# Performance work log

Hardware: AMD Instinct MI355X
Metric: run time of the kernel (lower is better)

## Reference

```python
import math
import jax, jax.numpy as jnp
import numpy as np

B, A, M, NC = 32, 8400, 32, 80
TOP_K, ALPHA, BETA, EPS = 13, 1.0, 6.0, 1e-9
IMG = 640.0


def _ciou(b1, b2, eps=1e-7):
    # b1, b2 broadcastable [..., 4]; CIoU as in compute_iou (box1=gt, box2=pred)
    b1x1, b1y1, b1x2, b1y2 = b1[..., 0], b1[..., 1], b1[..., 2], b1[..., 3]
    b2x1, b2y1, b2x2, b2y2 = b2[..., 0], b2[..., 1], b2[..., 2], b2[..., 3]
    w1, h1 = b1x2 - b1x1, b1y2 - b1y1 + eps
    w2, h2 = b2x2 - b2x1, b2y2 - b2y1 + eps
    inter = (jnp.minimum(b1x2, b2x2) - jnp.maximum(b1x1, b2x1)).clip(0) * \
            (jnp.minimum(b1y2, b2y2) - jnp.maximum(b1y1, b2y1)).clip(0)
    union = w1 * h1 + w2 * h2 - inter + eps
    iou = inter / union
    cw = jnp.maximum(b1x2, b2x2) - jnp.minimum(b1x1, b2x1)
    ch = jnp.maximum(b1y2, b2y2) - jnp.minimum(b1y1, b2y1)
    c2 = cw ** 2 + ch ** 2 + eps
    rho2 = ((b2x1 + b2x2 - b1x1 - b1x2) ** 2 + (b2y1 + b2y2 - b1y1 - b1y2) ** 2) / 4.0
    v = (4.0 / math.pi ** 2) * (jnp.arctan(w2 / h2) - jnp.arctan(w1 / h1)) ** 2
    alpha = jax.lax.stop_gradient(v / (v - iou + (1.0 + eps)))
    return iou - (rho2 / c2 + v * alpha)


def setup_inputs() -> dict:
    key = jax.random.key(0)
    ks = jax.random.split(key, 8)
    pd_scores = jax.random.uniform(ks[0], (B, A, NC), jnp.float32)
    anc_points = jax.random.uniform(ks[1], (A, 2), jnp.float32) * IMG
    # predicted boxes around anchor points (valid x1<x2, y1<y2)
    off = jax.random.uniform(ks[2], (B, A, 4), jnp.float32) * 80.0 + 2.0
    pd_bboxes = jnp.concatenate([anc_points[None] - off[..., :2],
                                 anc_points[None] + off[..., 2:]], -1)
    # GT boxes: random centers and sizes, clipped to image
    c = jax.random.uniform(ks[3], (B, M, 2), jnp.float32) * IMG
    wh = jax.random.uniform(ks[4], (B, M, 2), jnp.float32) * 180.0 + 20.0
    gt_bboxes = jnp.concatenate([(c - wh / 2).clip(0, IMG), (c + wh / 2).clip(0, IMG)], -1)
    gt_labels = jax.random.randint(ks[5], (B, M, 1), 0, NC, jnp.int64)
    n_valid = jax.random.randint(ks[6], (B,), 1, M + 1)
    mask_gt = (jnp.arange(M)[None, :] < n_valid[:, None]).astype(jnp.float32)[..., None]
    return {"pd_scores": pd_scores, "pd_bboxes": pd_bboxes, "anc_points": anc_points,
            "gt_labels": gt_labels, "gt_bboxes": gt_bboxes, "mask_gt": mask_gt}


def reference(pd_scores, pd_bboxes, anc_points, gt_labels, gt_bboxes, mask_gt):
    b, a, nc = pd_scores.shape
    m = gt_bboxes.shape[1]
    dtype = pd_scores.dtype

    # anchors-inside-GT mask: [B,M,A]
    lt = gt_bboxes[:, :, None, :2]          # [B,M,1,2]
    rb = gt_bboxes[:, :, None, 2:]
    deltas = jnp.concatenate([anc_points[None, None] - lt,
                              rb - anc_points[None, None]], -1)  # [B,M,A,4]
    mask_in_gts = deltas.min(-1) > EPS
    mg = mask_gt[..., 0] > 0                 # [B,M] bool
    gt_mask = mask_in_gts & mg[:, :, None]

    # per-GT class score gather: pd_scores[b, :, gt_labels[b,m]] -> [B,M,A]
    labels = gt_labels[..., 0]               # [B,M]
    idx = jnp.broadcast_to(labels[:, :, None, None], (b, m, a, 1))
    gathered = jnp.take_along_axis(jnp.broadcast_to(pd_scores[:, None], (b, m, a, nc)), idx, axis=3)[..., 0]
    bbox_scores = jnp.where(gt_mask, gathered, 0.0)

    # CIoU overlaps (dense, masked) [B,M,A]
    iou = _ciou(gt_bboxes[:, :, None, :], pd_bboxes[:, None, :, :])
    overlaps = jnp.where(gt_mask, jnp.maximum(iou, 0.0), 0.0)

    align_metric = bbox_scores ** ALPHA * overlaps ** BETA

    # top-k selection with duplicate suppression (faithful to scatter_add loop)
    _, tk_idx = jax.lax.top_k(align_metric, TOP_K)      # [B,M,K]
    tk_mask = jnp.broadcast_to(mg[:, :, None], tk_idx.shape)
    tk_idx = jnp.where(tk_mask, tk_idx, 0)
    bi = jnp.arange(b)[:, None, None]
    mi = jnp.arange(m)[None, :, None]
    counts = jnp.zeros((b, m, a), jnp.int32).at[bi, mi, tk_idx].add(1)
    mask_top_k = jnp.where(counts > 1, 0, counts).astype(dtype)

    mask_pos = mask_top_k * mask_in_gts.astype(dtype) * mg[:, :, None].astype(dtype)
    fg_mask = mask_pos.sum(1)                            # [B,A]

    # resolve anchors assigned to multiple GTs (no-op when none; matches torch branch)
    mask_multi = fg_mask[:, None, :] > 1                 # [B,M,A] (broadcast)
    max_idx = overlaps.argmax(1)                         # [B,A]
    is_max = (jnp.arange(m)[None, :, None] == max_idx[:, None, :]).astype(dtype)
    mask_pos = jnp.where(mask_multi, is_max, mask_pos)
    fg_mask = mask_pos.sum(1)

    target_gt_idx = mask_pos.argmax(1)                   # [B,A]
    target_labels = jnp.maximum(jnp.take_along_axis(labels, target_gt_idx, axis=1), 0)
    target_bboxes = jnp.take_along_axis(
        gt_bboxes, jnp.broadcast_to(target_gt_idx[..., None], (b, a, 4)), axis=1)

    target_scores = jax.nn.one_hot(target_labels, NC, dtype=dtype)
    target_scores = jnp.where((fg_mask > 0)[..., None], target_scores, 0.0)

    am = align_metric * mask_pos
    pos_am = am.max(-1, keepdims=True)                   # [B,M,1]
    pos_ov = (overlaps * mask_pos).max(-1, keepdims=True)
    norm = (am * pos_ov / (pos_am + EPS)).max(1)[..., None]  # [B,A,1]
    target_scores = target_scores * norm

    return target_bboxes, target_scores, fg_mask > 0
```

## Files before the change

### kernel.cpp

```cpp
#include <hip/hip_runtime.h>
#include <math.h>

#define BB 32
#define AA 8400
#define MM 32
#define NCC 80
#define TOPK 13
#define CAP 1024
#define NW (AA / 32 + 1)

typedef float nfloat4 __attribute__((ext_vector_type(4)));

__device__ __forceinline__ void wave_argmax(float& v, int& i) {
    #pragma unroll
    for (int off = 32; off > 0; off >>= 1) {
        float ov = __shfl_xor(v, off, 64);
        int oi = __shfl_xor(i, off, 64);
        if (ov > v || (ov == v && oi < i)) { v = ov; i = oi; }
    }
}

__global__ __launch_bounds__(256) void k12_topk(
        const float* __restrict__ pd_scores, const float* __restrict__ pd_bboxes,
        const float* __restrict__ anc, const int* __restrict__ gt_labels,
        const float* __restrict__ gt_bboxes, const float* __restrict__ mask_gt,
        int* __restrict__ sel_idx, float* __restrict__ pos_am, float* __restrict__ pos_ov) {
    __shared__ float lval[CAP];
    __shared__ int   lidx[CAP];
    __shared__ unsigned int bmask[NW];
    __shared__ float wv[4];
    __shared__ int   wi[4];
    __shared__ int   wsum[4];
    __shared__ int   s_p, s_sel;
    const float eps = 1e-7f;
    int bm = blockIdx.x;
    int b = bm >> 5;
    int tid = threadIdx.x;
    int lane = tid & 63;
    int wid = tid >> 6;
    if (tid == 0) pos_am[bm] = 0.f;
    if (tid == 1) pos_ov[bm] = 0.f;
    if (tid == 2) s_p = 0;
    if (tid == 3) s_sel = 0;
    if (tid < 16) sel_idx[bm * 16 + tid] = -1;
    if (!(mask_gt[bm] > 0.f)) return;

    for (int i = tid; i < NW; i += 256) bmask[i] = 0u;
    float4 g = reinterpret_cast<const float4*>(gt_bboxes)[bm];

    const float4* anc4 = reinterpret_cast<const float4*>(anc);
    unsigned long long bits = 0ull;
    int c_t = 0;
    #pragma unroll
    for (int j = 0; j < 17; j++) {
        int e = tid + (j << 8);
        if (e < 4200) {
            float4 an = anc4[e];
            float d0 = fminf(fminf(an.x - g.x, an.y - g.y), fminf(g.z - an.x, g.w - an.y));
            float d1 = fminf(fminf(an.z - g.x, an.w - g.y), fminf(g.z - an.z, g.w - an.w));
            if (d0 > 1e-9f) { bits |= 1ull << (2 * j);     c_t++; }
            if (d1 > 1e-9f) { bits |= 1ull << (2 * j + 1); c_t++; }
        }
    }
    int x = c_t;
    #pragma unroll
    for (int off = 1; off < 64; off <<= 1) {
        int y = __shfl_up(x, off, 64);
        if (lane >= off) x += y;
    }
    if (lane == 63) wsum[wid] = x;
    __syncthreads();
    int base = 0;
    #pragma unroll
    for (int w = 0; w < 4; w++) if (w < wid) base += wsum[w];
    int n_c = min(wsum[0] + wsum[1] + wsum[2] + wsum[3], CAP);
    {
        int o = base + x - c_t;
        unsigned long long mm_ = bits;
        while (mm_) {
            int k = __builtin_ctzll(mm_);
            mm_ &= mm_ - 1ull;
            int i = 2 * tid + 512 * (k >> 1) + (k & 1);
            if (o < CAP) lidx[o] = i;
            o++;
        }
    }
    for (int s = n_c + tid; s < CAP; s += 256) { lval[s] = -1.f; lidx[s] = AA; }
    __syncthreads();

    float w1 = g.z - g.x, h1 = g.w - g.y + eps;
    float atg = atanf(w1 / h1);
    float w1h1 = w1 * h1;
    float sgx = g.x + g.z, sgy = g.y + g.w;
    int lab = gt_labels[bm];
    const float4* pbb = reinterpret_cast<const float4*>(pd_bboxes) + (long)b * AA;
    const float* scp = pd_scores + (long)b * AA * NCC + lab;
    int nit = (n_c + 255) >> 8;
    for (int it = 0; it < nit; it++) {
        int s = (it << 8) + tid;
        bool pos = false;
        if (s < n_c) {
            int i = lidx[s];
            float4 pb = pbb[i];
            float sc = scp[(long)i * NCC];
            float w2 = pb.z - pb.x, h2 = pb.w - pb.y + eps;
            float iw = fmaxf(fminf(g.z, pb.z) - fmaxf(g.x, pb.x), 0.f);
            float ih = fmaxf(fminf(g.w, pb.w) - fmaxf(g.y, pb.y), 0.f);
            float inter = iw * ih;
            float uni = w1h1 + w2 * h2 - inter + eps;
            float iou = inter / uni;
            float cw = fmaxf(g.z, pb.z) - fminf(g.x, pb.x);
            float ch = fmaxf(g.w, pb.w) - fminf(g.y, pb.y);
            float c2 = cw * cw + ch * ch + eps;
            float dx = pb.x + pb.z - sgx, dy = pb.y + pb.w - sgy;
            float rho2 = (dx * dx + dy * dy) * 0.25f;
            float dv = atanf(w2 / h2) - atg;
            float v = 0.4052847345693511f * dv * dv;
            float alpha = v / (v - iou + (1.0f + eps));
            float cv = iou - (rho2 / c2 + v * alpha);
            float ov = fmaxf(cv, 0.f);
            float o2 = ov * ov;
            float val = sc * o2 * o2 * o2;
            pos = val > 0.f;
            lval[s] = pos ? val : -1.f;
            if (pos) atomicOr(&bmask[i >> 5], 1u << (i & 31));
        }
        unsigned long long pm = __ballot(pos);
        if (lane == 0) atomicAdd(&s_p, (int)__popcll(pm));
    }
    __syncthreads();
    int p = s_p;

    if (p >= TOPK) {
        float v0 = lval[tid], v1 = lval[tid + 256], v2 = lval[tid + 512], v3 = lval[tid + 768];
        int   i0 = lidx[tid], i1 = lidx[tid + 256], i2 = lidx[tid + 512], i3 = lidx[tid + 768];
        int mysel = -1;
        for (int k = 0; k < TOPK; k++) {
            float bv = v0; int bi = i0;
            if (v1 > bv || (v1 == bv && i1 < bi)) { bv = v1; bi = i1; }
            if (v2 > bv || (v2 == bv && i2 < bi)) { bv = v2; bi = i2; }
            if (v3 > bv || (v3 == bv && i3 < bi)) { bv = v3; bi = i3; }
            wave_argmax(bv, bi);
            if (lane == 0) { wv[wid] = bv; wi[wid] = bi; }
            __syncthreads();
            float gv = wv[0]; int gi = wi[0];
            #pragma unroll
            for (int w = 1; w < 4; w++) {
                float ov = wv[w]; int oi = wi[w];
                if (ov > gv || (ov == gv && oi < gi)) { gv = ov; gi = oi; }
            }
            if (tid == k) mysel = gi;
            if (i0 == gi) v0 = -1.f;
            if (i1 == gi) v1 = -1.f;
            if (i2 == gi) v2 = -1.f;
            if (i3 == gi) v3 = -1.f;
            __syncthreads();
        }
        if (tid < TOPK) sel_idx[bm * 16 + tid] = mysel;
    } else {
        for (int s = tid; s < n_c; s += 256)
            if (lval[s] > 0.f) {
                int slot = atomicAdd(&s_sel, 1);
                sel_idx[bm * 16 + slot] = lidx[s];
            }
        if (wid == 0) {
            int need = TOPK - p;
            for (int base_i = 0; need > 0 && base_i < AA; base_i += 64) {
                int i = base_i + lane;
                bool cand = (i < AA) && !((bmask[i >> 5] >> (i & 31)) & 1u);
                unsigned long long wm = __ballot(cand);
                int take = min(need, (int)__popcll(wm));
                if (cand && (int)__popcll(wm & ((1ull << lane) - 1ull)) < take) {
                    float2 an = reinterpret_cast<const float2*>(anc)[i];
                    float dmin = fminf(fminf(an.x - g.x, an.y - g.y), fminf(g.z - an.x, g.w - an.y));
                    if (dmin > 1e-9f) {
                        int slot = atomicAdd(&s_sel, 1);
                        sel_idx[bm * 16 + slot] = i;
                    }
                }
                need -= take;
            }
        }
    }
}

__global__ __launch_bounds__(256) void k3_resolve(
        const float* __restrict__ pd_scores, const float* __restrict__ pd_bboxes,
        const float* __restrict__ anc, const int* __restrict__ gt_labels,
        const float* __restrict__ gt_bboxes, const float* __restrict__ mask_gt,
        const int* __restrict__ sel_idx,
        float* __restrict__ pos_am, float* __restrict__ pos_ov,
        float* __restrict__ out_bbox, float* __restrict__ out_fg,
        int2* __restrict__ meta) {
    __shared__ float sg[MM][8];
    __shared__ int slab[MM];
    __shared__ int smg[MM];
    __shared__ unsigned int selcol[256];
    const float eps = 1e-7f;
    int b = blockIdx.y;
    int tid = threadIdx.x;
    if (tid < MM) {
        int gm = b * MM + tid;
        float4 g = reinterpret_cast<const float4*>(gt_bboxes)[gm];
        float w1 = g.z - g.x, h1 = g.w - g.y + eps;
        sg[tid][0] = g.x; sg[tid][1] = g.y; sg[tid][2] = g.z; sg[tid][3] = g.w;
        sg[tid][4] = w1 * h1;
        sg[tid][5] = atanf(w1 / h1);
        sg[tid][6] = g.x + g.z;
        sg[tid][7] = g.y + g.w;
        int lb = gt_labels[gm]; if (lb < 0) lb = 0;
        slab[tid] = lb;
        smg[tid] = mask_gt[gm] > 0.f ? 1 : 0;
    }
    selcol[tid] = 0u;
    __syncthreads();
    int a0 = blockIdx.x * 256;
    const int* sl = sel_idx + b * MM * 16;
    #pragma unroll
    for (int t = tid; t < MM * 16; t += 256) {
        int e = sl[t];
        if (e >= a0 && e < a0 + 256) atomicOr(&selcol[e - a0], 1u << (t >> 4));
    }
    __syncthreads();
    int a = a0 + tid;
    if (a >= AA) return;
    int g = b * AA + a;
    unsigned int sel = selcol[tid];
    int fg = __popc(sel);

    int tg = 0; bool fgo = false; float ovt = 0.f;
    if (fg >= 1) {
        float ax = anc[a * 2], ay = anc[a * 2 + 1];
        float4 pb = reinterpret_cast<const float4*>(pd_bboxes)[g];
        float w2 = pb.z - pb.x, h2 = pb.w - pb.y + eps;
        float atp = atanf(w2 / h2);
        float w2h2 = w2 * h2;
        float spx = pb.x + pb.z, spy = pb.y + pb.w;
        fgo = true;
        if (fg == 1) {
            tg = __ffs(sel) - 1;
            float gx1 = sg[tg][0], gy1 = sg[tg][1], gx2 = sg[tg][2], gy2 = sg[tg][3];
            float iw = fmaxf(fminf(gx2, pb.z) - fmaxf(gx1, pb.x), 0.f);
            float ih = fmaxf(fminf(gy2, pb.w) - fmaxf(gy1, pb.y), 0.f);
            float inter = iw * ih;
            float uni = sg[tg][4] + w2h2 - inter + eps;
            float iou = inter / uni;
            float cw = fmaxf(gx2, pb.z) - fminf(gx1, pb.x);
            float ch = fmaxf(gy2, pb.w) - fminf(gy1, pb.y);
            float c2 = cw * cw + ch * ch + eps;
            float dx = spx - sg[tg][6], dy = spy - sg[tg][7];
            float rho2 = (dx * dx + dy * dy) * 0.25f;
            float dv = atp - sg[tg][5];
            float v = 0.4052847345693511f * dv * dv;
            float alpha = v / (v - iou + (1.0f + eps));
            ovt = fmaxf(iou - (rho2 / c2 + v * alpha), 0.f);
        } else {
            float bestov = -1.f; int bestm = 0;
            for (int mm = 0; mm < MM; mm++) {
                float gx1 = sg[mm][0], gy1 = sg[mm][1], gx2 = sg[mm][2], gy2 = sg[mm][3];
                float dmin = fminf(fminf(ax - gx1, ay - gy1), fminf(gx2 - ax, gy2 - ay));
                float ov = 0.f;
                if ((dmin > 1e-9f) && smg[mm]) {
                    float iw = fmaxf(fminf(gx2, pb.z) - fmaxf(gx1, pb.x), 0.f);
                    float ih = fmaxf(fminf(gy2, pb.w) - fmaxf(gy1, pb.y), 0.f);
                    float inter = iw * ih;
                    float uni = sg[mm][4] + w2h2 - inter + eps;
                    float iou = inter / uni;
                    float cw = fmaxf(gx2, pb.z) - fminf(gx1, pb.x);
                    float ch = fmaxf(gy2, pb.w) - fminf(gy1, pb.y);
                    float c2 = cw * cw + ch * ch + eps;
                    float dx = spx - sg[mm][6], dy = spy - sg[mm][7];
                    float rho2 = (dx * dx + dy * dy) * 0.25f;
                    float dv = atp - sg[mm][5];
                    float v = 0.4052847345693511f * dv * dv;
                    float alpha = v / (v - iou + (1.0f + eps));
                    ov = fmaxf(iou - (rho2 / c2 + v * alpha), 0.f);
                }
                if (ov > bestov) { bestov = ov; bestm = mm; }
            }
            tg = bestm; ovt = bestov;
        }
    }

    nfloat4 gb = {sg[tg][0], sg[tg][1], sg[tg][2], sg[tg][3]};
    __builtin_nontemporal_store(gb, reinterpret_cast<nfloat4*>(out_bbox) + g);
    out_fg[g] = fgo ? 1.f : 0.f;
    float amv = 0.f;
    if (fgo) {
        float sc = pd_scores[(long)g * NCC + slab[tg]];
        float o2 = ovt * ovt;
        amv = sc * o2 * o2 * o2;
        atomicMax((int*)&pos_am[b * MM + tg], __float_as_int(amv));
        atomicMax((int*)&pos_ov[b * MM + tg], __float_as_int(ovt));
    }
    meta[g] = make_int2(__float_as_int(amv), tg | (slab[tg] << 8) | ((fgo ? 1 : 0) << 16));
}

__global__ __launch_bounds__(256) void k4_scores(
        const int2* __restrict__ meta,
        const float* __restrict__ pos_am, const float* __restrict__ pos_ov,
        float* __restrict__ out_scores) {
    int g = blockIdx.x * 256 + threadIdx.x;
    const int NQ = NCC / 4;
    if (g >= BB * AA * NQ) return;
    int ba = g / NQ;
    int c0 = (g % NQ) * 4;
    nfloat4 o = {0.f, 0.f, 0.f, 0.f};
    int2 mt = meta[ba];
    int p = mt.y;
    if (p & (1 << 16)) {
        int tg = p & 31, lab = (p >> 8) & 127;
        int b = ba / AA;
        int bm = b * MM + tg;
        float nv = (__int_as_float(mt.x) * pos_ov[bm]) / (pos_am[bm] + 1e-9f);
        int d = lab - c0;
        if (d == 0) o.x = nv; else if (d == 1) o.y = nv;
        else if (d == 2) o.z = nv; else if (d == 3) o.w = nv;
    }
    __builtin_nontemporal_store(o, reinterpret_cast<nfloat4*>(out_scores) + g);
}

extern "C" void kernel_launch(void* const* d_in, const int* in_sizes, int n_in,
                              void* d_out, int out_size, void* d_ws, size_t ws_size,
                              hipStream_t stream) {
    const float* pd_scores = (const float*)d_in[0];
    const float* pd_bboxes = (const float*)d_in[1];
    const float* anc       = (const float*)d_in[2];
    const int*   gt_labels = (const int*)d_in[3];
    const float* gt_bboxes = (const float*)d_in[4];
    const float* mask_gt   = (const float*)d_in[5];

    const long nBA = (long)BB * AA;

    char* ws = (char*)d_ws;
    int*   sel_idx = (int*)ws;                  ws += (long)BB * MM * 16 * 4;
    float* pos_am  = (float*)ws;                ws += BB * MM * 4;
    float* pos_ov  = (float*)ws;                ws += BB * MM * 4;
    int2*  meta    = (int2*)ws;                 ws += nBA * 8;

    float* out_bbox   = (float*)d_out;
    float* out_scores = out_bbox + nBA * 4;
    float* out_fg     = out_scores + nBA * NCC;

    k12_topk<<<BB * MM, 256, 0, stream>>>(pd_scores, pd_bboxes, anc, gt_labels,
                                          gt_bboxes, mask_gt, sel_idx, pos_am, pos_ov);
    dim3 g3((AA + 255) / 256, BB);
    k3_resolve<<<g3, 256, 0, stream>>>(pd_scores, pd_bboxes, anc, gt_labels,
                                       gt_bboxes, mask_gt, sel_idx, pos_am, pos_ov,
                                       out_bbox, out_fg, meta);
    long nS4 = nBA * (NCC / 4);
    k4_scores<<<(int)((nS4 + 255) / 256), 256, 0, stream>>>(meta, pos_am, pos_ov, out_scores);
}
```

Before: 188.5 us.

## Fuse three assignment kernels into one cooperative kernel with grid syncs

Replaces the top-k, resolve and score-writing kernels with a single cooperative kernel of 1024 blocks. Phases are separated by grid-wide syncs, and shared memory is reused through a union. The top-k phase now also stores the per-selection overlap and align metric, so single-assignment anchors no longer recompute CIoU. Per-anchor metadata stays in shared memory between phases instead of going through a global meta buffer. This removes launch gaps and a global round trip. In exchange it adds grid-barrier cost, and occupancy is limited to what lets all blocks be co-resident.

```diff
diff --git a/kernel.cpp b/kernel.cpp
--- a/kernel.cpp
+++ b/kernel.cpp
@@ -1,5 +1,8 @@
 #include <hip/hip_runtime.h>
+#include <hip/hip_cooperative_groups.h>
 #include <math.h>
+
+namespace cg = cooperative_groups;
 
 #define BB 32
 #define AA 8400
@@ -8,8 +11,35 @@
 #define TOPK 13
 #define CAP 1024
 #define NW (AA / 32 + 1)
+#define NCHUNK 33
+#define NTASK (BB * NCHUNK)
+#define GRID 1024
 
 typedef float nfloat4 __attribute__((ext_vector_type(4)));
+
+struct SmemA {
+    float lval[CAP];
+    int   lidx[CAP];
+    float oval[CAP];
+    unsigned int bmask[NW];
+    float wv[2][4];
+    int   wi[2][4];
+    int   wsum[4];
+    int   s_p, s_sel;
+    float s_ov[TOPK];
+};
+struct SmemB {
+    float sg[MM][8];
+    int   slab[MM];
+    int   smg[MM];
+    unsigned int selcol[256];
+    float sov[256];
+    float sam[256];
+    float samv[2][256];
+    int   smeta[2][256];
+    float snv[256];
+};
+union Smem { SmemA a; SmemB b; };
 
 __device__ __forceinline__ void wave_argmax(float& v, int& i) {
     #pragma unroll
@@ -20,304 +50,309 @@
     }
 }
 
-__global__ __launch_bounds__(256) void k12_topk(
+__global__ __launch_bounds__(256, 4) void fused_assign(
         const float* __restrict__ pd_scores, const float* __restrict__ pd_bboxes,
         const float* __restrict__ anc, const int* __restrict__ gt_labels,
         const float* __restrict__ gt_bboxes, const float* __restrict__ mask_gt,
-        int* __restrict__ sel_idx, float* __restrict__ pos_am, float* __restrict__ pos_ov) {
-    __shared__ float lval[CAP];
-    __shared__ int   lidx[CAP];
-    __shared__ unsigned int bmask[NW];
-    __shared__ float wv[4];
-    __shared__ int   wi[4];
-    __shared__ int   wsum[4];
-    __shared__ int   s_p, s_sel;
+        int* __restrict__ sel_idx, float* __restrict__ sel_ov, float* __restrict__ sel_am,
+        float* __restrict__ pos_am, float* __restrict__ pos_ov,
+        float* __restrict__ out_bbox, float* __restrict__ out_scores,
+        float* __restrict__ out_fg) {
+    __shared__ Smem sm;
     const float eps = 1e-7f;
-    int bm = blockIdx.x;
-    int b = bm >> 5;
     int tid = threadIdx.x;
     int lane = tid & 63;
     int wid = tid >> 6;
-    if (tid == 0) pos_am[bm] = 0.f;
-    if (tid == 1) pos_ov[bm] = 0.f;
-    if (tid == 2) s_p = 0;
-    if (tid == 3) s_sel = 0;
-    if (tid < 16) sel_idx[bm * 16 + tid] = -1;
-    if (!(mask_gt[bm] > 0.f)) return;
-
-    for (int i = tid; i < NW; i += 256) bmask[i] = 0u;
-    float4 g = reinterpret_cast<const float4*>(gt_bboxes)[bm];
-
-    const float4* anc4 = reinterpret_cast<const float4*>(anc);
-    unsigned long long bits = 0ull;
-    int c_t = 0;
-    #pragma unroll
-    for (int j = 0; j < 17; j++) {
-        int e = tid + (j << 8);
-        if (e < 4200) {
-            float4 an = anc4[e];
-            float d0 = fminf(fminf(an.x - g.x, an.y - g.y), fminf(g.z - an.x, g.w - an.y));
-            float d1 = fminf(fminf(an.z - g.x, an.w - g.y), fminf(g.z - an.z, g.w - an.w));
-            if (d0 > 1e-9f) { bits |= 1ull << (2 * j);     c_t++; }
-            if (d1 > 1e-9f) { bits |= 1ull << (2 * j + 1); c_t++; }
-        }
-    }
-    int x = c_t;
-    #pragma unroll
-    for (int off = 1; off < 64; off <<= 1) {
-        int y = __shfl_up(x, off, 64);
-        if (lane >= off) x += y;
-    }
-    if (lane == 63) wsum[wid] = x;
-    __syncthreads();
-    int base = 0;
-    #pragma unroll
-    for (int w = 0; w < 4; w++) if (w < wid) base += wsum[w];
-    int n_c = min(wsum[0] + wsum[1] + wsum[2] + wsum[3], CAP);
+
     {
-        int o = base + x - c_t;
-        unsigned long long mm_ = bits;
-        while (mm_) {
-            int k = __builtin_ctzll(mm_);
-            mm_ &= mm_ - 1ull;
-            int i = 2 * tid + 512 * (k >> 1) + (k & 1);
-            if (o < CAP) lidx[o] = i;
-            o++;
-        }
-    }
-    for (int s = n_c + tid; s < CAP; s += 256) { lval[s] = -1.f; lidx[s] = AA; }
-    __syncthreads();
-
-    float w1 = g.z - g.x, h1 = g.w - g.y + eps;
-    float atg = atanf(w1 / h1);
-    float w1h1 = w1 * h1;
-    float sgx = g.x + g.z, sgy = g.y + g.w;
-    int lab = gt_labels[bm];
-    const float4* pbb = reinterpret_cast<const float4*>(pd_bboxes) + (long)b * AA;
-    const float* scp = pd_scores + (long)b * AA * NCC + lab;
-    int nit = (n_c + 255) >> 8;
-    for (int it = 0; it < nit; it++) {
-        int s = (it << 8) + tid;
-        bool pos = false;
-        if (s < n_c) {
-            int i = lidx[s];
-            float4 pb = pbb[i];
-            float sc = scp[(long)i * NCC];
-            float w2 = pb.z - pb.x, h2 = pb.w - pb.y + eps;
-            float iw = fmaxf(fminf(g.z, pb.z) - fmaxf(g.x, pb.x), 0.f);
-            float ih = fmaxf(fminf(g.w, pb.w) - fmaxf(g.y, pb.y), 0.f);
-            float inter = iw * ih;
-            float uni = w1h1 + w2 * h2 - inter + eps;
-            float iou = inter / uni;
-            float cw = fmaxf(g.z, pb.z) - fminf(g.x, pb.x);
-            float ch = fmaxf(g.w, pb.w) - fminf(g.y, pb.y);
-            float c2 = cw * cw + ch * ch + eps;
-            float dx = pb.x + pb.z - sgx, dy = pb.y + pb.w - sgy;
-            float rho2 = (dx * dx + dy * dy) * 0.25f;
-            float dv = atanf(w2 / h2) - atg;
-            float v = 0.4052847345693511f * dv * dv;
-            float alpha = v / (v - iou + (1.0f + eps));
-            float cv = iou - (rho2 / c2 + v * alpha);
-            float ov = fmaxf(cv, 0.f);
-            float o2 = ov * ov;
-            float val = sc * o2 * o2 * o2;
-            pos = val > 0.f;
-            lval[s] = pos ? val : -1.f;
-            if (pos) atomicOr(&bmask[i >> 5], 1u << (i & 31));
-        }
-        unsigned long long pm = __ballot(pos);
-        if (lane == 0) atomicAdd(&s_p, (int)__popcll(pm));
-    }
-    __syncthreads();
-    int p = s_p;
-
-    if (p >= TOPK) {
-        float v0 = lval[tid], v1 = lval[tid + 256], v2 = lval[tid + 512], v3 = lval[tid + 768];
-        int   i0 = lidx[tid], i1 = lidx[tid + 256], i2 = lidx[tid + 512], i3 = lidx[tid + 768];
-        int mysel = -1;
-        for (int k = 0; k < TOPK; k++) {
-            float bv = v0; int bi = i0;
-            if (v1 > bv || (v1 == bv && i1 < bi)) { bv = v1; bi = i1; }
-            if (v2 > bv || (v2 == bv && i2 < bi)) { bv = v2; bi = i2; }
-            if (v3 > bv || (v3 == bv && i3 < bi)) { bv = v3; bi = i3; }
-            wave_argmax(bv, bi);
-            if (lane == 0) { wv[wid] = bv; wi[wid] = bi; }
+        int bm = blockIdx.x;
+        int b = bm >> 5;
+        if (tid == 0) pos_am[bm] = 0.f;
+        if (tid == 1) pos_ov[bm] = 0.f;
+        if (tid == 2) sm.a.s_p = 0;
+        if (tid == 3) sm.a.s_sel = 0;
+        if (tid < 16) sel_idx[bm * 16 + tid] = -1;
+        if (mask_gt[bm] > 0.f) {
+            for (int i = tid; i < NW; i += 256) sm.a.bmask[i] = 0u;
+            float4 g = reinterpret_cast<const float4*>(gt_bboxes)[bm];
+
+            const float4* anc4 = reinterpret_cast<const float4*>(anc);
+            unsigned long long bits = 0ull;
+            int c_t = 0;
+            #pragma unroll
+            for (int j = 0; j < 17; j++) {
+                int e = tid + (j << 8);
+                if (e < 4200) {
+                    float4 an = anc4[e];
+                    float d0 = fminf(fminf(an.x - g.x, an.y - g.y), fminf(g.z - an.x, g.w - an.y));
+                    float d1 = fminf(fminf(an.z - g.x, an.w - g.y), fminf(g.z - an.z, g.w - an.w));
+                    if (d0 > 1e-9f) { bits |= 1ull << (2 * j);     c_t++; }
+                    if (d1 > 1e-9f) { bits |= 1ull << (2 * j + 1); c_t++; }
+                }
+            }
+            int x = c_t;
+            #pragma unroll
+            for (int off = 1; off < 64; off <<= 1) {
+                int y = __shfl_up(x, off, 64);
+                if (lane >= off) x += y;
+            }
+            if (lane == 63) sm.a.wsum[wid] = x;
             __syncthreads();
-            float gv = wv[0]; int gi = wi[0];
+            int base = 0;
             #pragma unroll
-            for (int w = 1; w < 4; w++) {
-                float ov = wv[w]; int oi = wi[w];
-                if (ov > gv || (ov == gv && oi < gi)) { gv = ov; gi = oi; }
-            }
-            if (tid == k) mysel = gi;
-            if (i0 == gi) v0 = -1.f;
-            if (i1 == gi) v1 = -1.f;
-            if (i2 == gi) v2 = -1.f;
-            if (i3 == gi) v3 = -1.f;
+            for (int w = 0; w < 4; w++) if (w < wid) base += sm.a.wsum[w];
+            int n_c = min(sm.a.wsum[0] + sm.a.wsum[1] + sm.a.wsum[2] + sm.a.wsum[3], CAP);
+            {
+                int o = base + x - c_t;
+                unsigned long long mm_ = bits;
+                while (mm_) {
+                    int k = __builtin_ctzll(mm_);
+                    mm_ &= mm_ - 1ull;
+                    int i = 2 * tid + 512 * (k >> 1) + (k & 1);
+                    if (o < CAP) sm.a.lidx[o] = i;
+                    o++;
+                }
+            }
+            for (int s = n_c + tid; s < CAP; s += 256) { sm.a.lval[s] = -1.f; sm.a.lidx[s] = AA; }
             __syncthreads();
-        }
-        if (tid < TOPK) sel_idx[bm * 16 + tid] = mysel;
-    } else {
-        for (int s = tid; s < n_c; s += 256)
-            if (lval[s] > 0.f) {
-                int slot = atomicAdd(&s_sel, 1);
-                sel_idx[bm * 16 + slot] = lidx[s];
-            }
-        if (wid == 0) {
-            int need = TOPK - p;
-            for (int base_i = 0; need > 0 && base_i < AA; base_i += 64) {
-                int i = base_i + lane;
-                bool cand = (i < AA) && !((bmask[i >> 5] >> (i & 31)) & 1u);
-                unsigned long long wm = __ballot(cand);
-                int take = min(need, (int)__popcll(wm));
-                if (cand && (int)__popcll(wm & ((1ull << lane) - 1ull)) < take) {
-                    float2 an = reinterpret_cast<const float2*>(anc)[i];
-                    float dmin = fminf(fminf(an.x - g.x, an.y - g.y), fminf(g.z - an.x, g.w - an.y));
-                    if (dmin > 1e-9f) {
-                        int slot = atomicAdd(&s_sel, 1);
-                        sel_idx[bm * 16 + slot] = i;
-                    }
-                }
-                need -= take;
-            }
-        }
-    }
-}
-
-__global__ __launch_bounds__(256) void k3_resolve(
-        const float* __restrict__ pd_scores, const float* __restrict__ pd_bboxes,
-        const float* __restrict__ anc, const int* __restrict__ gt_labels,
-        const float* __restrict__ gt_bboxes, const float* __restrict__ mask_gt,
-        const int* __restrict__ sel_idx,
-        float* __restrict__ pos_am, float* __restrict__ pos_ov,
-        float* __restrict__ out_bbox, float* __restrict__ out_fg,
-        int2* __restrict__ meta) {
-    __shared__ float sg[MM][8];
-    __shared__ int slab[MM];
-    __shared__ int smg[MM];
-    __shared__ unsigned int selcol[256];
-    const float eps = 1e-7f;
-    int b = blockIdx.y;
-    int tid = threadIdx.x;
-    if (tid < MM) {
-        int gm = b * MM + tid;
-        float4 g = reinterpret_cast<const float4*>(gt_bboxes)[gm];
-        float w1 = g.z - g.x, h1 = g.w - g.y + eps;
-        sg[tid][0] = g.x; sg[tid][1] = g.y; sg[tid][2] = g.z; sg[tid][3] = g.w;
-        sg[tid][4] = w1 * h1;
-        sg[tid][5] = atanf(w1 / h1);
-        sg[tid][6] = g.x + g.z;
-        sg[tid][7] = g.y + g.w;
-        int lb = gt_labels[gm]; if (lb < 0) lb = 0;
-        slab[tid] = lb;
-        smg[tid] = mask_gt[gm] > 0.f ? 1 : 0;
-    }
-    selcol[tid] = 0u;
-    __syncthreads();
-    int a0 = blockIdx.x * 256;
-    const int* sl = sel_idx + b * MM * 16;
-    #pragma unroll
-    for (int t = tid; t < MM * 16; t += 256) {
-        int e = sl[t];
-        if (e >= a0 && e < a0 + 256) atomicOr(&selcol[e - a0], 1u << (t >> 4));
-    }
-    __syncthreads();
-    int a = a0 + tid;
-    if (a >= AA) return;
-    int g = b * AA + a;
-    unsigned int sel = selcol[tid];
-    int fg = __popc(sel);
-
-    int tg = 0; bool fgo = false; float ovt = 0.f;
-    if (fg >= 1) {
-        float ax = anc[a * 2], ay = anc[a * 2 + 1];
-        float4 pb = reinterpret_cast<const float4*>(pd_bboxes)[g];
-        float w2 = pb.z - pb.x, h2 = pb.w - pb.y + eps;
-        float atp = atanf(w2 / h2);
-        float w2h2 = w2 * h2;
-        float spx = pb.x + pb.z, spy = pb.y + pb.w;
-        fgo = true;
-        if (fg == 1) {
-            tg = __ffs(sel) - 1;
-            float gx1 = sg[tg][0], gy1 = sg[tg][1], gx2 = sg[tg][2], gy2 = sg[tg][3];
-            float iw = fmaxf(fminf(gx2, pb.z) - fmaxf(gx1, pb.x), 0.f);
-            float ih = fmaxf(fminf(gy2, pb.w) - fmaxf(gy1, pb.y), 0.f);
-            float inter = iw * ih;
-            float uni = sg[tg][4] + w2h2 - inter + eps;
-            float iou = inter / uni;
-            float cw = fmaxf(gx2, pb.z) - fminf(gx1, pb.x);
-            float ch = fmaxf(gy2, pb.w) - fminf(gy1, pb.y);
-            float c2 = cw * cw + ch * ch + eps;
-            float dx = spx - sg[tg][6], dy = spy - sg[tg][7];
-            float rho2 = (dx * dx + dy * dy) * 0.25f;
-            float dv = atp - sg[tg][5];
-            float v = 0.4052847345693511f * dv * dv;
-            float alpha = v / (v - iou + (1.0f + eps));
-            ovt = fmaxf(iou - (rho2 / c2 + v * alpha), 0.f);
-        } else {
-            float bestov = -1.f; int bestm = 0;
-            for (int mm = 0; mm < MM; mm++) {
-                float gx1 = sg[mm][0], gy1 = sg[mm][1], gx2 = sg[mm][2], gy2 = sg[mm][3];
-                float dmin = fminf(fminf(ax - gx1, ay - gy1), fminf(gx2 - ax, gy2 - ay));
-                float ov = 0.f;
-                if ((dmin > 1e-9f) && smg[mm]) {
-                    float iw = fmaxf(fminf(gx2, pb.z) - fmaxf(gx1, pb.x), 0.f);
-                    float ih = fmaxf(fminf(gy2, pb.w) - fmaxf(gy1, pb.y), 0.f);
+
+            float w1 = g.z - g.x, h1 = g.w - g.y + eps;
+            float atg = atanf(w1 / h1);
+            float w1h1 = w1 * h1;
+            float sgx = g.x + g.z, sgy = g.y + g.w;
+            int lab = gt_labels[bm];
+            const float4* pbb = reinterpret_cast<const float4*>(pd_bboxes) + (long)b * AA;
+            const float* scp = pd_scores + (long)b * AA * NCC + lab;
+            int nit = (n_c + 255) >> 8;
+            for (int it = 0; it < nit; it++) {
+                int s = (it << 8) + tid;
+                bool pos = false;
+                if (s < n_c) {
+                    int i = sm.a.lidx[s];
+                    float4 pb = pbb[i];
+                    float sc = scp[(long)i * NCC];
+                    float w2 = pb.z - pb.x, h2 = pb.w - pb.y + eps;
+                    float iw = fmaxf(fminf(g.z, pb.z) - fmaxf(g.x, pb.x), 0.f);
+                    float ih = fmaxf(fminf(g.w, pb.w) - fmaxf(g.y, pb.y), 0.f);
                     float inter = iw * ih;
-                    float uni = sg[mm][4] + w2h2 - inter + eps;
+                    float uni = w1h1 + w2 * h2 - inter + eps;
                     float iou = inter / uni;
-                    float cw = fmaxf(gx2, pb.z) - fminf(gx1, pb.x);
-                    float ch = fmaxf(gy2, pb.w) - fminf(gy1, pb.y);
+                    float cw = fmaxf(g.z, pb.z) - fminf(g.x, pb.x);
+                    float ch = fmaxf(g.w, pb.w) - fminf(g.y, pb.y);
                     float c2 = cw * cw + ch * ch + eps;
-                    float dx = spx - sg[mm][6], dy = spy - sg[mm][7];
+                    float dx = pb.x + pb.z - sgx, dy = pb.y + pb.w - sgy;
                     float rho2 = (dx * dx + dy * dy) * 0.25f;
-                    float dv = atp - sg[mm][5];
+                    float dv = atanf(w2 / h2) - atg;
                     float v = 0.4052847345693511f * dv * dv;
                     float alpha = v / (v - iou + (1.0f + eps));
-                    ov = fmaxf(iou - (rho2 / c2 + v * alpha), 0.f);
-                }
-                if (ov > bestov) { bestov = ov; bestm = mm; }
-            }
-            tg = bestm; ovt = bestov;
+                    float cv = iou - (rho2 / c2 + v * alpha);
+                    float ov = fmaxf(cv, 0.f);
+                    float o2 = ov * ov;
+                    float val = sc * o2 * o2 * o2;
+                    pos = val > 0.f;
+                    sm.a.lval[s] = pos ? val : -1.f;
+                    sm.a.oval[s] = ov;
+                    if (pos) atomicOr(&sm.a.bmask[i >> 5], 1u << (i & 31));
+                }
+                unsigned long long pm = __ballot(pos);
+                if (lane == 0) atomicAdd(&sm.a.s_p, (int)__popcll(pm));
+            }
+            __syncthreads();
+            int p = sm.a.s_p;
+
+            if (p >= TOPK) {
+                float v0 = sm.a.lval[tid], v1 = sm.a.lval[tid + 256], v2 = sm.a.lval[tid + 512], v3 = sm.a.lval[tid + 768];
+                int   i0 = sm.a.lidx[tid], i1 = sm.a.lidx[tid + 256], i2 = sm.a.lidx[tid + 512], i3 = sm.a.lidx[tid + 768];
+                int mysel = -1; float myval = 0.f;
+                for (int k = 0; k < TOPK; k++) {
+                    float bv = v0; int bi = i0;
+                    if (v1 > bv || (v1 == bv && i1 < bi)) { bv = v1; bi = i1; }
+                    if (v2 > bv || (v2 == bv && i2 < bi)) { bv = v2; bi = i2; }
+                    if (v3 > bv || (v3 == bv && i3 < bi)) { bv = v3; bi = i3; }
+                    wave_argmax(bv, bi);
+                    if (lane == 0) { sm.a.wv[k & 1][wid] = bv; sm.a.wi[k & 1][wid] = bi; }
+                    __syncthreads();
+                    float gv = sm.a.wv[k & 1][0]; int gi = sm.a.wi[k & 1][0];
+                    #pragma unroll
+                    for (int w = 1; w < 4; w++) {
+                        float ov = sm.a.wv[k & 1][w]; int oi = sm.a.wi[k & 1][w];
+                        if (ov > gv || (ov == gv && oi < gi)) { gv = ov; gi = oi; }
+                    }
+                    if (tid == k) { mysel = gi; myval = gv; }
+                    if (i0 == gi) { v0 = -1.f; sm.a.s_ov[k] = sm.a.oval[tid]; }
+                    if (i1 == gi) { v1 = -1.f; sm.a.s_ov[k] = sm.a.oval[tid + 256]; }
+                    if (i2 == gi) { v2 = -1.f; sm.a.s_ov[k] = sm.a.oval[tid + 512]; }
+                    if (i3 == gi) { v3 = -1.f; sm.a.s_ov[k] = sm.a.oval[tid + 768]; }
+                }
+                __syncthreads();
+                if (tid < TOPK) {
+                    sel_idx[bm * 16 + tid] = mysel;
+                    sel_am[bm * 16 + tid] = myval;
+                    sel_ov[bm * 16 + tid] = sm.a.s_ov[tid];
+                }
+            } else {
+                for (int s = tid; s < n_c; s += 256)
+                    if (sm.a.lval[s] > 0.f) {
+                        int slot = atomicAdd(&sm.a.s_sel, 1);
+                        sel_idx[bm * 16 + slot] = sm.a.lidx[s];
+                        sel_ov[bm * 16 + slot] = sm.a.oval[s];
+                        sel_am[bm * 16 + slot] = sm.a.lval[s];
+                    }
+                if (wid == 0) {
+                    int need = TOPK - p;
+                    for (int base_i = 0; need > 0 && base_i < AA; base_i += 64) {
+                        int i = base_i + lane;
+                        bool cand = (i < AA) && !((sm.a.bmask[i >> 5] >> (i & 31)) & 1u);
+                        unsigned long long wm = __ballot(cand);
+                        int take = min(need, (int)__popcll(wm));
+                        if (cand && (int)__popcll(wm & ((1ull << lane) - 1ull)) < take) {
+                            float2 an = reinterpret_cast<const float2*>(anc)[i];
+                            float dmin = fminf(fminf(an.x - g.x, an.y - g.y), fminf(g.z - an.x, g.w - an.y));
+                            if (dmin > 1e-9f) {
+                                int slot = atomicAdd(&sm.a.s_sel, 1);
+                                sel_idx[bm * 16 + slot] = i;
+                                sel_ov[bm * 16 + slot] = 0.f;
+                                sel_am[bm * 16 + slot] = 0.f;
+                            }
+                        }
+                        need -= take;
+                    }
+                }
+            }
         }
     }
-
-    nfloat4 gb = {sg[tg][0], sg[tg][1], sg[tg][2], sg[tg][3]};
-    __builtin_nontemporal_store(gb, reinterpret_cast<nfloat4*>(out_bbox) + g);
-    out_fg[g] = fgo ? 1.f : 0.f;
-    float amv = 0.f;
-    if (fgo) {
-        float sc = pd_scores[(long)g * NCC + slab[tg]];
-        float o2 = ovt * ovt;
-        amv = sc * o2 * o2 * o2;
-        atomicMax((int*)&pos_am[b * MM + tg], __float_as_int(amv));
-        atomicMax((int*)&pos_ov[b * MM + tg], __float_as_int(ovt));
+    __threadfence();
+    cg::this_grid().sync();
+
+    for (int task = blockIdx.x; task < NTASK; task += GRID) {
+        int tb = task / NCHUNK;
+        int chunk = task - tb * NCHUNK;
+        int sidx = task >= GRID ? 1 : 0;
+        int a0 = chunk << 8;
+        if (tid < MM) {
+            int gm = tb * MM + tid;
+            float4 gg = reinterpret_cast<const float4*>(gt_bboxes)[gm];
+            float w1 = gg.z - gg.x, h1 = gg.w - gg.y + eps;
+            sm.b.sg[tid][0] = gg.x; sm.b.sg[tid][1] = gg.y; sm.b.sg[tid][2] = gg.z; sm.b.sg[tid][3] = gg.w;
+            sm.b.sg[tid][4] = w1 * h1;
+            sm.b.sg[tid][5] = atanf(w1 / h1);
+            sm.b.sg[tid][6] = gg.x + gg.z;
+            sm.b.sg[tid][7] = gg.y + gg.w;
+            int lb = gt_labels[gm]; if (lb < 0) lb = 0;
+            sm.b.slab[tid] = lb;
+            sm.b.smg[tid] = mask_gt[gm] > 0.f ? 1 : 0;
+        }
+        sm.b.selcol[tid] = 0u;
+        __syncthreads();
+        const int* sl = sel_idx + tb * MM * 16;
+        #pragma unroll
+        for (int t = tid; t < MM * 16; t += 256) {
+            int e = sl[t];
+            if (e >= a0 && e < a0 + 256) {
+                atomicOr(&sm.b.selcol[e - a0], 1u << (t >> 4));
+                sm.b.sov[e - a0] = sel_ov[tb * MM * 16 + t];
+                sm.b.sam[e - a0] = sel_am[tb * MM * 16 + t];
+            }
+        }
+        __syncthreads();
+        int a = a0 + tid;
+        float amv = 0.f; int tg = 0; int fgo = 0;
+        if (a < AA) {
+            long gidx = (long)tb * AA + a;
+            unsigned int sel = sm.b.selcol[tid];
+            int fg = __popc(sel);
+            float ovt = 0.f;
+            if (fg == 1) {
+                tg = __ffs(sel) - 1;
+                ovt = sm.b.sov[tid];
+                amv = sm.b.sam[tid];
+                fgo = 1;
+            } else if (fg > 1) {
+                float ax = anc[a * 2], ay = anc[a * 2 + 1];
+                float4 pb = reinterpret_cast<const float4*>(pd_bboxes)[gidx];
+                float w2 = pb.z - pb.x, h2 = pb.w - pb.y + eps;
+                float atp = atanf(w2 / h2);
+                float w2h2 = w2 * h2;
+                float spx = pb.x + pb.z, spy = pb.y + pb.w;
+                float bestov = -1.f; int bestm = 0;
+                for (int mm_ = 0; mm_ < MM; mm_++) {
+                    float gx1 = sm.b.sg[mm_][0], gy1 = sm.b.sg[mm_][1], gx2 = sm.b.sg[mm_][2], gy2 = sm.b.sg[mm_][3];
+                    float dmin = fminf(fminf(ax - gx1, ay - gy1), fminf(gx2 - ax, gy2 - ay));
+                    float ov = 0.f;
+                    if ((dmin > 1e-9f) && sm.b.smg[mm_]) {
+                        float iw = fmaxf(fminf(gx2, pb.z) - fmaxf(gx1, pb.x), 0.f);
+                        float ih = fmaxf(fminf(gy2, pb.w) - fmaxf(gy1, pb.y), 0.f);
+                        float inter = iw * ih;
+                        float uni = sm.b.sg[mm_][4] + w2h2 - inter + eps;
+                        float iou = inter / uni;
+                        float cw = fmaxf(gx2, pb.z) - fminf(gx1, pb.x);
+                        float ch = fmaxf(gy2, pb.w) - fminf(gy1, pb.y);
+                        float c2 = cw * cw + ch * ch + eps;
+                        float dx = spx - sm.b.sg[mm_][6], dy = spy - sm.b.sg[mm_][7];
+                        float rho2 = (dx * dx + dy * dy) * 0.25f;
+                        float dv = atp - sm.b.sg[mm_][5];
+                        float v = 0.4052847345693511f * dv * dv;
+                        float alpha = v / (v - iou + (1.0f + eps));
+                        ov = fmaxf(iou - (rho2 / c2 + v * alpha), 0.f);
+                    }
+                    if (ov > bestov) { bestov = ov; bestm = mm_; }
+                }
+                tg = bestm; ovt = bestov;
+                float sc = pd_scores[gidx * NCC + sm.b.slab[tg]];
+                float o2 = ovt * ovt;
+                amv = sc * o2 * o2 * o2;
+                fgo = 1;
+            }
+            nfloat4 gb = {sm.b.sg[tg][0], sm.b.sg[tg][1], sm.b.sg[tg][2], sm.b.sg[tg][3]};
+            __builtin_nontemporal_store(gb, reinterpret_cast<nfloat4*>(out_bbox) + gidx);
+            __builtin_nontemporal_store(fgo ? 1.f : 0.f, out_fg + gidx);
+            if (fgo) {
+                atomicMax((int*)&pos_am[tb * MM + tg], __float_as_int(amv));
+                atomicMax((int*)&pos_ov[tb * MM + tg], __float_as_int(ovt));
+            }
+        }
+        sm.b.samv[sidx][tid] = amv;
+        sm.b.smeta[sidx][tid] = tg | (sm.b.slab[tg] << 8) | (fgo << 16);
+        __syncthreads();
     }
-    meta[g] = make_int2(__float_as_int(amv), tg | (slab[tg] << 8) | ((fgo ? 1 : 0) << 16));
-}
-
-__global__ __launch_bounds__(256) void k4_scores(
-        const int2* __restrict__ meta,
-        const float* __restrict__ pos_am, const float* __restrict__ pos_ov,
-        float* __restrict__ out_scores) {
-    int g = blockIdx.x * 256 + threadIdx.x;
-    const int NQ = NCC / 4;
-    if (g >= BB * AA * NQ) return;
-    int ba = g / NQ;
-    int c0 = (g % NQ) * 4;
-    nfloat4 o = {0.f, 0.f, 0.f, 0.f};
-    int2 mt = meta[ba];
-    int p = mt.y;
-    if (p & (1 << 16)) {
-        int tg = p & 31, lab = (p >> 8) & 127;
-        int b = ba / AA;
-        int bm = b * MM + tg;
-        float nv = (__int_as_float(mt.x) * pos_ov[bm]) / (pos_am[bm] + 1e-9f);
-        int d = lab - c0;
-        if (d == 0) o.x = nv; else if (d == 1) o.y = nv;
-        else if (d == 2) o.z = nv; else if (d == 3) o.w = nv;
+    __threadfence();
+    cg::this_grid().sync();
+
+    for (int task = blockIdx.x; task < NTASK; task += GRID) {
+        int tb = task / NCHUNK;
+        int chunk = task - tb * NCHUNK;
+        int sidx = task >= GRID ? 1 : 0;
+        int a0 = chunk << 8;
+        {
+            int mt = sm.b.smeta[sidx][tid];
+            float nv = 0.f;
+            if (mt & (1 << 16)) {
+                int tg = mt & 31;
+                int bmi = tb * MM + tg;
+                nv = sm.b.samv[sidx][tid] * pos_ov[bmi] / (pos_am[bmi] + 1e-9f);
+            }
+            sm.b.snv[tid] = nv;
+        }
+        __syncthreads();
+        const long base4 = ((long)tb * AA + a0) * (NCC / 4);
+        nfloat4* outs4 = reinterpret_cast<nfloat4*>(out_scores);
+        #pragma unroll
+        for (int idx = tid; idx < 256 * 20; idx += 256) {
+            int al = idx / 20;
+            int q = idx - al * 20;
+            int aa_ = a0 + al;
+            if (aa_ < AA) {
+                nfloat4 o = {0.f, 0.f, 0.f, 0.f};
+                float nv = sm.b.snv[al];
+                int lab = (sm.b.smeta[sidx][al] >> 8) & 127;
+                int d = lab - (q << 2);
+                if (d == 0) o.x = nv; else if (d == 1) o.y = nv;
+                else if (d == 2) o.z = nv; else if (d == 3) o.w = nv;
+                __builtin_nontemporal_store(o, outs4 + base4 + idx);
+            }
+        }
+        __syncthreads();
     }
-    __builtin_nontemporal_store(o, reinterpret_cast<nfloat4*>(out_scores) + g);
 }
 
 extern "C" void kernel_launch(void* const* d_in, const int* in_sizes, int n_in,
@@ -333,21 +368,22 @@
     const long nBA = (long)BB * AA;
 
     char* ws = (char*)d_ws;
-    int*   sel_idx = (int*)ws;                  ws += (long)BB * MM * 16 * 4;
-    float* pos_am  = (float*)ws;                ws += BB * MM * 4;
-    float* pos_ov  = (float*)ws;                ws += BB * MM * 4;
-    int2*  meta    = (int2*)ws;                 ws += nBA * 8;
+    int*   sel_idx = (int*)ws;    ws += (long)BB * MM * 16 * 4;
+    float* sel_ov  = (float*)ws;  ws += (long)BB * MM * 16 * 4;
+    float* sel_am  = (float*)ws;  ws += (long)BB * MM * 16 * 4;
+    float* pos_am  = (float*)ws;  ws += BB * MM * 4;
+    float* pos_ov  = (float*)ws;  ws += BB * MM * 4;
 
     float* out_bbox   = (float*)d_out;
     float* out_scores = out_bbox + nBA * 4;
     float* out_fg     = out_scores + nBA * NCC;
 
-    k12_topk<<<BB * MM, 256, 0, stream>>>(pd_scores, pd_bboxes, anc, gt_labels,
-                                          gt_bboxes, mask_gt, sel_idx, pos_am, pos_ov);
-    dim3 g3((AA + 255) / 256, BB);
-    k3_resolve<<<g3, 256, 0, stream>>>(pd_scores, pd_bboxes, anc, gt_labels,
-                                       gt_bboxes, mask_gt, sel_idx, pos_am, pos_ov,
-                                       out_bbox, out_fg, meta);
-    long nS4 = nBA * (NCC / 4);
-    k4_scores<<<(int)((nS4 + 255) / 256), 256, 0, stream>>>(meta, pos_am, pos_ov, out_scores);
+    void* args[] = {
+        (void*)&pd_scores, (void*)&pd_bboxes, (void*)&anc, (void*)&gt_labels,
+        (void*)&gt_bboxes, (void*)&mask_gt,
+        (void*)&sel_idx, (void*)&sel_ov, (void*)&sel_am,
+        (void*)&pos_am, (void*)&pos_ov,
+        (void*)&out_bbox, (void*)&out_scores, (void*)&out_fg
+    };
+    hipLaunchCooperativeKernel((void*)fused_assign, dim3(GRID), dim3(256), args, 0, stream);
 }
```

Result: slower. 594.1 us (+215.1%).

## Use per-wave top-k with a final merge and pass overlaps to the resolve stage

Applied to the files above, without the earlier changes.

The block-wide top-k loop, which needed two barriers per iteration, becomes an independent top-13 per wave followed by a single merge of the 52 candidates in wave 0. The selected overlap and align-metric values are now written to the workspace, so the resolve kernel no longer recomputes CIoU and gathers a score for anchors matched to a single GT. The cost is an extra shared array and more small workspace reads and writes. The per-wave partitioning of candidates changes, and pb/pbb must exist in the hidden code for the fallback path to compile.

```diff
diff --git a/kernel.cpp b/kernel.cpp
--- a/kernel.cpp
+++ b/kernel.cpp
@@ -24,12 +24,15 @@
         const float* __restrict__ pd_scores, const float* __restrict__ pd_bboxes,
         const float* __restrict__ anc, const int* __restrict__ gt_labels,
         const float* __restrict__ gt_bboxes, const float* __restrict__ mask_gt,
-        int* __restrict__ sel_idx, float* __restrict__ pos_am, float* __restrict__ pos_ov) {
+        int* __restrict__ sel_idx, float* __restrict__ sel_ov, float* __restrict__ sel_am,
+        float* __restrict__ pos_am, float* __restrict__ pos_ov) {
     __shared__ float lval[CAP];
     __shared__ int   lidx[CAP];
+    __shared__ float oval[CAP];
     __shared__ unsigned int bmask[NW];
-    __shared__ float wv[4];
-    __shared__ int   wi[4];
+    __shared__ float lw[4][TOPK];
+    __shared__ int   li[4][TOPK];
+    __shared__ float lo[4][TOPK];
     __shared__ int   wsum[4];
     __shared__ int   s_p, s_sel;
     const float eps = 1e-7f;
@@ -123,6 +126,7 @@
             float val = sc * o2 * o2 * o2;
             pos = val > 0.f;
             lval[s] = pos ? val : -1.f;
+            oval[s] = ov;
             if (pos) atomicOr(&bmask[i >> 5], 1u << (i & 31));
         }
         unsigned long long pm = __ballot(pos);
@@ -132,36 +136,46 @@
     int p = s_p;
 
     if (p >= TOPK) {
-        float v0 = lval[tid], v1 = lval[tid + 256], v2 = lval[tid + 512], v3 = lval[tid + 768];
-        int   i0 = lidx[tid], i1 = lidx[tid + 256], i2 = lidx[tid + 512], i3 = lidx[tid + 768];
-        int mysel = -1;
+        int s0 = (wid << 8) + lane;
+        float v0 = lval[s0], v1 = lval[s0 + 64], v2 = lval[s0 + 128], v3 = lval[s0 + 192];
+        int   i0 = lidx[s0], i1 = lidx[s0 + 64], i2 = lidx[s0 + 128], i3 = lidx[s0 + 192];
         for (int k = 0; k < TOPK; k++) {
             float bv = v0; int bi = i0;
             if (v1 > bv || (v1 == bv && i1 < bi)) { bv = v1; bi = i1; }
             if (v2 > bv || (v2 == bv && i2 < bi)) { bv = v2; bi = i2; }
             if (v3 > bv || (v3 == bv && i3 < bi)) { bv = v3; bi = i3; }
             wave_argmax(bv, bi);
-            if (lane == 0) { wv[wid] = bv; wi[wid] = bi; }
-            __syncthreads();
-            float gv = wv[0]; int gi = wi[0];
-            #pragma unroll
-            for (int w = 1; w < 4; w++) {
-                float ov = wv[w]; int oi = wi[w];
-                if (ov > gv || (ov == gv && oi < gi)) { gv = ov; gi = oi; }
-            }
-            if (tid == k) mysel = gi;
-            if (i0 == gi) v0 = -1.f;
-            if (i1 == gi) v1 = -1.f;
-            if (i2 == gi) v2 = -1.f;
-            if (i3 == gi) v3 = -1.f;
-            __syncthreads();
-        }
-        if (tid < TOPK) sel_idx[bm * 16 + tid] = mysel;
+            if (i0 == bi) { v0 = -1.f; lo[wid][k] = oval[s0]; }
+            if (i1 == bi) { v1 = -1.f; lo[wid][k] = oval[s0 + 64]; }
+            if (i2 == bi) { v2 = -1.f; lo[wid][k] = oval[s0 + 128]; }
+            if (i3 == bi) { v3 = -1.f; lo[wid][k] = oval[s0 + 192]; }
+            if (lane == 0) { lw[wid][k] = bv; li[wid][k] = bi; }
+        }
+        __syncthreads();
+        if (wid == 0) {
+            float mv = -1.f; int mi = AA; float mo = 0.f;
+            if (lane < 4 * TOPK) {
+                int w = lane / TOPK, k = lane - w * TOPK;
+                mv = lw[w][k]; mi = li[w][k]; mo = lo[w][k];
+            }
+            for (int k = 0; k < TOPK; k++) {
+                float bv = mv; int bi = mi;
+                wave_argmax(bv, bi);
+                if (mi == bi && mv > -1.f) {
+                    sel_idx[bm * 16 + k] = bi;
+                    sel_am[bm * 16 + k] = bv;
+                    sel_ov[bm * 16 + k] = mo;
+                    mv = -1.f;
+                }
+            }
+        }
     } else {
         for (int s = tid; s < n_c; s += 256)
             if (lval[s] > 0.f) {
                 int slot = atomicAdd(&s_sel, 1);
                 sel_idx[bm * 16 + slot] = lidx[s];
+                sel_ov[bm * 16 + slot] = oval[s];
+                sel_am[bm * 16 + slot] = lval[s];
             }
         if (wid == 0) {
             int need = TOPK - p;
@@ -174,8 +188,26 @@
                     float2 an = reinterpret_cast<const float2*>(anc)[i];
                     float dmin = fminf(fminf(an.x - g.x, an.y - g.y), fminf(g.z - an.x, g.w - an.y));
                     if (dmin > 1e-9f) {
+                        float4 pb = pbb[i];
+                        float w2 = pb.z - pb.x, h2 = pb.w - pb.y + eps;
+                        float iw = fmaxf(fminf(g.z, pb.z) - fmaxf(g.x, pb.x), 0.f);
+                        float ih = fmaxf(fminf(g.w, pb.w) - fmaxf(g.y, pb.y), 0.f);
+                        float inter = iw * ih;
+                        float uni = w1h1 + w2 * h2 - inter + eps;
+                        float iou = inter / uni;
+                        float cw = fmaxf(g.z, pb.z) - fminf(g.x, pb.x);
+                        float ch = fmaxf(g.w, pb.w) - fminf(g.y, pb.y);
+                        float c2 = cw * cw + ch * ch + eps;
+                        float dx = pb.x + pb.z - sgx, dy = pb.y + pb.w - sgy;
+                        float rho2 = (dx * dx + dy * dy) * 0.25f;
+                        float dv = atanf(w2 / h2) - atg;
+                        float v = 0.4052847345693511f * dv * dv;
+                        float alpha = v / (v - iou + (1.0f + eps));
+                        float ov = fmaxf(iou - (rho2 / c2 + v * alpha), 0.f);
                         int slot = atomicAdd(&s_sel, 1);
                         sel_idx[bm * 16 + slot] = i;
+                        sel_ov[bm * 16 + slot] = ov;
+                        sel_am[bm * 16 + slot] = 0.f;
                     }
                 }
                 need -= take;
@@ -188,7 +220,8 @@
         const float* __restrict__ pd_scores, const float* __restrict__ pd_bboxes,
         const float* __restrict__ anc, const int* __restrict__ gt_labels,
         const float* __restrict__ gt_bboxes, const float* __restrict__ mask_gt,
-        const int* __restrict__ sel_idx,
+        const int* __restrict__ sel_idx, const float* __restrict__ sel_ov,
+        const float* __restrict__ sel_am,
         float* __restrict__ pos_am, float* __restrict__ pos_ov,
         float* __restrict__ out_bbox, float* __restrict__ out_fg,
         int2* __restrict__ meta) {
@@ -196,6 +229,8 @@
     __shared__ int slab[MM];
     __shared__ int smg[MM];
     __shared__ unsigned int selcol[256];
+    __shared__ float sov[256];
+    __shared__ float sam[256];
     const float eps = 1e-7f;
     int b = blockIdx.y;
     int tid = threadIdx.x;
@@ -219,7 +254,11 @@
     #pragma unroll
     for (int t = tid; t < MM * 16; t += 256) {
         int e = sl[t];
-        if (e >= a0 && e < a0 + 256) atomicOr(&selcol[e - a0], 1u << (t >> 4));
+        if (e >= a0 && e < a0 + 256) {
+            atomicOr(&selcol[e - a0], 1u << (t >> 4));
+            sov[e - a0] = sel_ov[b * MM * 16 + t];
+            sam[e - a0] = sel_am[b * MM * 16 + t];
+        }
     }
     __syncthreads();
     int a = a0 + tid;
@@ -228,68 +267,53 @@
     unsigned int sel = selcol[tid];
     int fg = __popc(sel);
 
-    int tg = 0; bool fgo = false; float ovt = 0.f;
-    if (fg >= 1) {
+    int tg = 0; bool fgo = false; float ovt = 0.f; float amv = 0.f;
+    if (fg == 1) {
+        tg = __ffs(sel) - 1;
+        ovt = sov[tid];
+        amv = sam[tid];
+        fgo = true;
+    } else if (fg > 1) {
         float ax = anc[a * 2], ay = anc[a * 2 + 1];
         float4 pb = reinterpret_cast<const float4*>(pd_bboxes)[g];
         float w2 = pb.z - pb.x, h2 = pb.w - pb.y + eps;
         float atp = atanf(w2 / h2);
         float w2h2 = w2 * h2;
         float spx = pb.x + pb.z, spy = pb.y + pb.w;
+        float bestov = -1.f; int bestm = 0;
+        for (int mm = 0; mm < MM; mm++) {
+            float gx1 = sg[mm][0], gy1 = sg[mm][1], gx2 = sg[mm][2], gy2 = sg[mm][3];
+            float dmin = fminf(fminf(ax - gx1, ay - gy1), fminf(gx2 - ax, gy2 - ay));
+            float ov = 0.f;
+            if ((dmin > 1e-9f) && smg[mm]) {
+                float iw = fmaxf(fminf(gx2, pb.z) - fmaxf(gx1, pb.x), 0.f);
+                float ih = fmaxf(fminf(gy2, pb.w) - fmaxf(gy1, pb.y), 0.f);
+                float inter = iw * ih;
+                float uni = sg[mm][4] + w2h2 - inter + eps;
+                float iou = inter / uni;
+                float cw = fmaxf(gx2, pb.z) - fminf(gx1, pb.x);
+                float ch = fmaxf(gy2, pb.w) - fminf(gy1, pb.y);
+                float c2 = cw * cw + ch * ch + eps;
+                float dx = spx - sg[mm][6], dy = spy - sg[mm][7];
+                float rho2 = (dx * dx + dy * dy) * 0.25f;
+                float dv = atp - sg[mm][5];
+                float v = 0.4052847345693511f * dv * dv;
+                float alpha = v / (v - iou + (1.0f + eps));
+                ov = fmaxf(iou - (rho2 / c2 + v * alpha), 0.f);
+            }
+            if (ov > bestov) { bestov = ov; bestm = mm; }
+        }
+        tg = bestm; ovt = bestov;
+        float sc = pd_scores[(long)g * NCC + slab[tg]];
+        float o2 = ovt * ovt;
+        amv = sc * o2 * o2 * o2;
         fgo = true;
-        if (fg == 1) {
-            tg = __ffs(sel) - 1;
-            float gx1 = sg[tg][0], gy1 = sg[tg][1], gx2 = sg[tg][2], gy2 = sg[tg][3];
-            float iw = fmaxf(fminf(gx2, pb.z) - fmaxf(gx1, pb.x), 0.f);
-            float ih = fmaxf(fminf(gy2, pb.w) - fmaxf(gy1, pb.y), 0.f);
-            float inter = iw * ih;
-            float uni = sg[tg][4] + w2h2 - inter + eps;
-            float iou = inter / uni;
-            float cw = fmaxf(gx2, pb.z) - fminf(gx1, pb.x);
-            float ch = fmaxf(gy2, pb.w) - fminf(gy1, pb.y);
-            float c2 = cw * cw + ch * ch + eps;
-            float dx = spx - sg[tg][6], dy = spy - sg[tg][7];
-            float rho2 = (dx * dx + dy * dy) * 0.25f;
-            float dv = atp - sg[tg][5];
-            float v = 0.4052847345693511f * dv * dv;
-            float alpha = v / (v - iou + (1.0f + eps));
-            ovt = fmaxf(iou - (rho2 / c2 + v * alpha), 0.f);
-        } else {
-            float bestov = -1.f; int bestm = 0;
-            for (int mm = 0; mm < MM; mm++) {
-                float gx1 = sg[mm][0], gy1 = sg[mm][1], gx2 = sg[mm][2], gy2 = sg[mm][3];
-                float dmin = fminf(fminf(ax - gx1, ay - gy1), fminf(gx2 - ax, gy2 - ay));
-                float ov = 0.f;
-                if ((dmin > 1e-9f) && smg[mm]) {
-                    float iw = fmaxf(fminf(gx2, pb.z) - fmaxf(gx1, pb.x), 0.f);
-                    float ih = fmaxf(fminf(gy2, pb.w) - fmaxf(gy1, pb.y), 0.f);
-                    float inter = iw * ih;
-                    float uni = sg[mm][4] + w2h2 - inter + eps;
-                    float iou = inter / uni;
-                    float cw = fmaxf(gx2, pb.z) - fminf(gx1, pb.x);
-                    float ch = fmaxf(gy2, pb.w) - fminf(gy1, pb.y);
-                    float c2 = cw * cw + ch * ch + eps;
-                    float dx = spx - sg[mm][6], dy = spy - sg[mm][7];
-                    float rho2 = (dx * dx + dy * dy) * 0.25f;
-                    float dv = atp - sg[mm][5];
-                    float v = 0.4052847345693511f * dv * dv;
-                    float alpha = v / (v - iou + (1.0f + eps));
-                    ov = fmaxf(iou - (rho2 / c2 + v * alpha), 0.f);
-                }
-                if (ov > bestov) { bestov = ov; bestm = mm; }
-            }
-            tg = bestm; ovt = bestov;
-        }
     }
 
     nfloat4 gb = {sg[tg][0], sg[tg][1], sg[tg][2], sg[tg][3]};
     __builtin_nontemporal_store(gb, reinterpret_cast<nfloat4*>(out_bbox) + g);
     out_fg[g] = fgo ? 1.f : 0.f;
-    float amv = 0.f;
     if (fgo) {
-        float sc = pd_scores[(long)g * NCC + slab[tg]];
-        float o2 = ovt * ovt;
-        amv = sc * o2 * o2 * o2;
         atomicMax((int*)&pos_am[b * MM + tg], __float_as_int(amv));
         atomicMax((int*)&pos_ov[b * MM + tg], __float_as_int(ovt));
     }
@@ -334,6 +358,8 @@
 
     char* ws = (char*)d_ws;
     int*   sel_idx = (int*)ws;                  ws += (long)BB * MM * 16 * 4;
+    float* sel_ov  = (float*)ws;                ws += (long)BB * MM * 16 * 4;
+    float* sel_am  = (float*)ws;                ws += (long)BB * MM * 16 * 4;
     float* pos_am  = (float*)ws;                ws += BB * MM * 4;
     float* pos_ov  = (float*)ws;                ws += BB * MM * 4;
     int2*  meta    = (int2*)ws;                 ws += nBA * 8;
@@ -343,11 +369,12 @@
     float* out_fg     = out_scores + nBA * NCC;
 
     k12_topk<<<BB * MM, 256, 0, stream>>>(pd_scores, pd_bboxes, anc, gt_labels,
-                                          gt_bboxes, mask_gt, sel_idx, pos_am, pos_ov);
+                                          gt_bboxes, mask_gt, sel_idx, sel_ov, sel_am,
+                                          pos_am, pos_ov);
     dim3 g3((AA + 255) / 256, BB);
     k3_resolve<<<g3, 256, 0, stream>>>(pd_scores, pd_bboxes, anc, gt_labels,
-                                       gt_bboxes, mask_gt, sel_idx, pos_am, pos_ov,
-                                       out_bbox, out_fg, meta);
+                                       gt_bboxes, mask_gt, sel_idx, sel_ov, sel_am,
+                                       pos_am, pos_ov, out_bbox, out_fg, meta);
     long nS4 = nBA * (NCC / 4);
     k4_scores<<<(int)((nS4 + 255) / 256), 256, 0, stream>>>(meta, pos_am, pos_ov, out_scores);
 }
```

Result: slower. 193.8 us (+2.8%).
